# Performance work log

Hardware: AMD Instinct MI355X
Metric: run time of the kernel (lower is better)

The kernel has to match this reference:

```python
import jax, jax.numpy as jnp
import numpy as np

N, T, D, H = 256, 128, 512, 1024


def setup_inputs() -> dict:
    key = jax.random.key(0)
    k_x, k_A, k_Wx, k_Wh, k_Wa = jax.random.split(key, 5)
    x = jax.random.normal(k_x, (N, T, D), dtype=jnp.float32)
    A = jax.random.normal(k_A, (N, H, 4, 4), dtype=jnp.float32)
    Wx = jax.random.normal(k_Wx, (D, 4 * H), dtype=jnp.float32) / np.sqrt(D)
    Wh = jax.random.normal(k_Wh, (H, 4 * H), dtype=jnp.float32) / np.sqrt(H)
    Wattn = jax.random.normal(k_Wa, (H, 4 * H), dtype=jnp.float32) / np.sqrt(H)
    b = jnp.zeros((4 * H,), dtype=jnp.float32)
    return {"x": x, "A": A, "Wx": Wx, "Wh": Wh, "Wattn": Wattn, "b": b}


def _attention_lstm(x, A, Wx, Wh, Wattn, b):
    # A: (N, H, 4, 4) -> flatten spatial to (N, H, 16)
    A_flat = A.reshape(A.shape[0], A.shape[1], -1)
    h0 = A_flat.mean(axis=2)  # (N, H)
    c0 = h0
    Hdim = h0.shape[1]
    scale = 1.0 / jnp.sqrt(jnp.asarray(Hdim, dtype=x.dtype))

    def step(carry, x_t):
        prev_h, prev_c = carry
        # scaled dot-product attention over 16 spatial locations
        scores = jnp.einsum("nh,nhs->ns", prev_h, A_flat) * scale  # (N, 16)
        w = jax.nn.softmax(scores, axis=1)
        attn = jnp.einsum("nhs,ns->nh", A_flat, w)  # (N, H)
        # fused LSTM gates
        a = x_t @ Wx + prev_h @ Wh + attn @ Wattn + b  # (N, 4H)
        i = jax.nn.sigmoid(a[:, 0:Hdim])
        f = jax.nn.sigmoid(a[:, Hdim:2 * Hdim])
        o = jax.nn.sigmoid(a[:, 2 * Hdim:3 * Hdim])
        g = jnp.tanh(a[:, 3 * Hdim:4 * Hdim])
        next_c = f * prev_c + i * g
        next_h = o * jnp.tanh(next_c)
        return (next_h, next_c), next_h

    x_tnd = jnp.swapaxes(x, 0, 1)  # (T, N, D)
    _, h_tnh = jax.lax.scan(step, (h0, c0), x_tnd)
    return jnp.swapaxes(h_tnh, 0, 1)  # (N, T, H)


def reference(x, A, Wx, Wh, Wattn, b):
    return _attention_lstm(x, A, Wx, Wh, Wattn, b)
```

## Files before the change

kernel.cpp:

```cpp
#include <hip/hip_runtime.h>
#include <math.h>

#define NB 256
#define TT 128
#define DD 512
#define HH 1024
#define KHX 1536
#define KFB 2560
#define BK 128
#define NBLK7 256
#define HSLOT (NB * HH)
#define SCSLOT2 (NB * 16)

typedef _Float16 half_t;
typedef _Float16 half8 __attribute__((ext_vector_type(8)));
typedef _Float16 half4v __attribute__((ext_vector_type(4)));
typedef _Float16 half2v __attribute__((ext_vector_type(2)));
typedef float f32x4 __attribute__((ext_vector_type(4)));


__global__ __launch_bounds__(256) void k_trans(const float* __restrict__ src,
        half_t* __restrict__ dst, int kstride, int koff, int nkt) {
    __shared__ half_t tile[64][65];
    int bk = blockIdx.x % nkt;
    int bn = blockIdx.x / nkt;
    int k0 = bk * 64, n0 = bn * 64;
    #pragma unroll
    for (int i = 0; i < 16; ++i) {
        int idx = i * 256 + threadIdx.x;
        int r = idx >> 6, c = idx & 63;
        tile[c][r] = (half_t)src[(size_t)(k0 + r) * 4096 + n0 + c];
    }
    __syncthreads();
    #pragma unroll
    for (int i = 0; i < 16; ++i) {
        int idx = i * 256 + threadIdx.x;
        int r = idx >> 6, c = idx & 63;
        dst[(size_t)(n0 + r) * kstride + koff + k0 + c] = tile[r][c];
    }
}

__global__ __launch_bounds__(256) void k_convA2(const float* __restrict__ A,
        half_t* __restrict__ A16, half_t* __restrict__ AsT,
        float* __restrict__ cbuf, half_t* __restrict__ h16) {
    int n = blockIdx.x, tid = threadIdx.x;
    #pragma unroll
    for (int r = 0; r < 4; ++r) {
        int h = tid + r * 256;
        const float4* ap = (const float4*)(A + ((size_t)n * HH + h) * 16);
        float4 v0 = ap[0], v1 = ap[1], v2 = ap[2], v3 = ap[3];
        float a[16];
        a[0]=v0.x; a[1]=v0.y; a[2] =v0.z; a[3] =v0.w;
        a[4]=v1.x; a[5]=v1.y; a[6] =v1.z; a[7] =v1.w;
        a[8]=v2.x; a[9]=v2.y; a[10]=v2.z; a[11]=v2.w;
        a[12]=v3.x; a[13]=v3.y; a[14]=v3.z; a[15]=v3.w;
        float hv = 0.f;
        #pragma unroll
        for (int s = 0; s < 16; ++s) hv += a[s];
        hv *= (1.f / 16.f);
        size_t ci = (size_t)n * HH + h;
        cbuf[ci] = hv;
        h16[ci] = (half_t)hv;
        half8 q0, q1;
        #pragma unroll
        for (int s = 0; s < 8; ++s) { q0[s] = (half_t)a[s]; q1[s] = (half_t)a[s + 8]; }
        *(half8*)(A16 + ci * 16) = q0;
        *(half8*)(A16 + ci * 16 + 8) = q1;
        #pragma unroll
        for (int s = 0; s < 16; ++s)
            AsT[(size_t)n * 16 * HH + (size_t)s * HH + h] = (half_t)a[s];
    }
}

__global__ __launch_bounds__(256) void k_gemm_G(const half_t* __restrict__ AsT,
        const half_t* __restrict__ WaT, half_t* __restrict__ G16) {
    __shared__ half_t sAs[16][BK + 8];
    __shared__ half_t sB[4][16][BK + 8];
    int bid = blockIdx.x;
    int n = bid >> 6, jt = bid & 63;
    int j0 = jt * 16;
    int tid = threadIdx.x, wv = tid >> 6, lane = tid & 63;
    f32x4 acc = {};
    int srB = tid >> 2, scB = (tid & 3) * 32;
    int gB = srB >> 4, jcB = srB & 15;
    for (int it = 0; it < HH / BK; ++it) {
        int k0 = it * BK;
        if (tid < 128) {
            int r = tid >> 3, c = (tid & 7) * 16;
            const uint4* sp = (const uint4*)(AsT + (size_t)n * 16 * HH + (size_t)r * HH + k0 + c);
            uint4 u0 = sp[0], u1 = sp[1];
            *(uint4*)&sAs[r][c] = u0;
            *(uint4*)&sAs[r][c + 8] = u1;
        }
        {
            const half_t* src = WaT + ((size_t)(gB * HH + j0 + jcB)) * HH + k0 + scB;
            uint4 u0 = ((const uint4*)src)[0];
            uint4 u1 = ((const uint4*)src)[1];
            uint4 u2 = ((const uint4*)src)[2];
            uint4 u3 = ((const uint4*)src)[3];
            *((uint4*)&sB[gB][jcB][scB])      = u0;
            *((uint4*)&sB[gB][jcB][scB + 8])  = u1;
            *((uint4*)&sB[gB][jcB][scB + 16]) = u2;
            *((uint4*)&sB[gB][jcB][scB + 24]) = u3;
        }
        __syncthreads();
        int row16 = lane & 15, kg = lane >> 4;
        #pragma unroll
        for (int kc = 0; kc < BK / 32; ++kc) {
            half8 bf = *(const half8*)&sB[wv][row16][kc * 32 + kg * 8];
            half8 af = *(const half8*)&sAs[row16][kc * 32 + kg * 8];
            acc = __builtin_amdgcn_mfma_f32_16x16x32_f16(af, bf, acc, 0, 0, 0);
        }
        __syncthreads();
    }
    int col = lane & 15, rbase = (lane >> 4) * 4;
    size_t jf = (size_t)wv * HH + j0 + col;
    half4v o;
    o[0] = (half_t)acc[0]; o[1] = (half_t)acc[1];
    o[2] = (half_t)acc[2]; o[3] = (half_t)acc[3];
    *(half4v*)(G16 + ((size_t)n * 4096 + jf) * 16 + rbase) = o;
}

__global__ __launch_bounds__(256) void k_gemm_XW4(const float* __restrict__ x,
        const half_t* __restrict__ WhxT, half_t* __restrict__ XW16) {
    __shared__ half_t sA[128][72];
    __shared__ half_t sB[128][72];
    int bid = blockIdx.x;
    int bm = bid >> 5;
    int bj = bid & 31;
    int row0 = bm * 128;
    int col0 = bj * 128;
    int tid = threadIdx.x, wv = tid >> 6, lane = tid & 63;
    int la = lane & 15, kg = lane >> 4;
    int mh = wv & 1, jh = wv >> 1;
    f32x4 acc[4][4] = {};
    int rs = tid >> 1, seg = (tid & 1) * 32;
    for (int c = 0; c < 8; ++c) {
        {
            const float4* sp = (const float4*)(x + (size_t)(row0 + rs) * DD + c * 64 + seg);
            half8 p0, p1, p2, p3;
            float4 u0 = sp[0], u1 = sp[1], u2 = sp[2], u3 = sp[3];
            float4 u4 = sp[4], u5 = sp[5], u6 = sp[6], u7 = sp[7];
            p0[0]=(half_t)u0.x; p0[1]=(half_t)u0.y; p0[2]=(half_t)u0.z; p0[3]=(half_t)u0.w;
            p0[4]=(half_t)u1.x; p0[5]=(half_t)u1.y; p0[6]=(half_t)u1.z; p0[7]=(half_t)u1.w;
            p1[0]=(half_t)u2.x; p1[1]=(half_t)u2.y; p1[2]=(half_t)u2.z; p1[3]=(half_t)u2.w;
            p1[4]=(half_t)u3.x; p1[5]=(half_t)u3.y; p1[6]=(half_t)u3.z; p1[7]=(half_t)u3.w;
            p2[0]=(half_t)u4.x; p2[1]=(half_t)u4.y; p2[2]=(half_t)u4.z; p2[3]=(half_t)u4.w;
            p2[4]=(half_t)u5.x; p2[5]=(half_t)u5.y; p2[6]=(half_t)u5.z; p2[7]=(half_t)u5.w;
            p3[0]=(half_t)u6.x; p3[1]=(half_t)u6.y; p3[2]=(half_t)u6.z; p3[3]=(half_t)u6.w;
            p3[4]=(half_t)u7.x; p3[5]=(half_t)u7.y; p3[6]=(half_t)u7.z; p3[7]=(half_t)u7.w;
            *(half8*)&sA[rs][seg]      = p0;
            *(half8*)&sA[rs][seg + 8]  = p1;
            *(half8*)&sA[rs][seg + 16] = p2;
            *(half8*)&sA[rs][seg + 24] = p3;
        }
        {
            const uint4* sp = (const uint4*)(WhxT + (size_t)(col0 + rs) * KHX + c * 64 + seg);
            uint4 u0 = sp[0], u1 = sp[1];
            *(uint4*)&sB[rs][seg]     = u0;
            *(uint4*)&sB[rs][seg + 8] = u1;
        }
        __syncthreads();
        #pragma unroll
        for (int ks = 0; ks < 2; ++ks) {
            half8 bfr[4];
            #pragma unroll
            for (int jt = 0; jt < 4; ++jt)
                bfr[jt] = *(const half8*)&sB[jh * 64 + jt * 16 + la][ks * 32 + kg * 8];
            #pragma unroll
            for (int m = 0; m < 4; ++m) {
                half8 af = *(const half8*)&sA[mh * 64 + m * 16 + la][ks * 32 + kg * 8];
                #pragma unroll
                for (int jt = 0; jt < 4; ++jt)
                    acc[m][jt] = __builtin_amdgcn_mfma_f32_16x16x32_f16(af, bfr[jt], acc[m][jt], 0, 0, 0);
            }
        }
        __syncthreads();
    }
    #pragma unroll
    for (int ch = 0; ch < 2; ++ch) {
        __syncthreads();
        if (jh == ch) {
            #pragma unroll
            for (int m = 0; m < 4; ++m)
                #pragma unroll
                for (int jt = 0; jt < 4; ++jt)
                    #pragma unroll
                    for (int q = 0; q < 4; ++q)
                        sB[mh * 64 + m * 16 + kg * 4 + q][jt * 16 + la] =
                            (half_t)acc[m][jt][q];
        }
        __syncthreads();
        int cbase = col0 + ch * 64;
        int g = cbase >> 10;
        int jbb = (cbase & 1023) >> 3;
        #pragma unroll
        for (int i = 0; i < 4; ++i) {
            int idx = tid + i * 256;
            int rl = idx >> 3, grp = idx & 7;
            int R = row0 + rl;
            int t = R & 127, nn = R >> 7;
            int mh2 = nn >> 7, nl2 = nn & 127;
            size_t dst = ((((size_t)t * 128 + (jbb + grp)) * 2 + mh2) * 128 + nl2) * 32 + g * 8;
            *(half8*)(XW16 + dst) = *(const half8*)&sB[rl][grp * 8];
        }
    }
}


__global__ __launch_bounds__(512, 1) void k_steps7(
        const half_t* __restrict__ XW16, half_t* __restrict__ hh,
        const half_t* __restrict__ WhxT, const half_t* __restrict__ A16,
        const half_t* __restrict__ G16, const float* __restrict__ b,
        const float* __restrict__ cbuf, float* __restrict__ scr,
        float* __restrict__ out, int* __restrict__ bar) {
    __shared__ half_t W[32][1028];
    __shared__ float red[8][16];
    __shared__ float pe[128][33];

    int bid = blockIdx.x;
    int mhalf = bid & 1, jb = bid >> 1;
    int n0 = mhalf * 128;
    int tid = threadIdx.x;
    int wvi = tid >> 6, lane = tid & 63;
    int la = lane & 15, kg = lane >> 4;
    int* hcnt = bar + mhalf * 32;
    int* scnt = bar + 64 + mhalf * 32;

    {
        int wr = tid >> 4, seg = tid & 15;
        const half_t* wsrc = WhxT + (size_t)((wr >> 3) * HH + jb * 8 + (wr & 7)) * KHX
                           + DD + seg * 64;
        #pragma unroll
        for (int i = 0; i < 8; ++i)
            *(uint4*)&W[wr][seg * 64 + i * 8] = ((const uint4*)wsrc)[i];
    }

    int n_l = tid & 127, jg2 = tid >> 7;
    int n = n0 + n_l;
    int n_home = n0 + jb;
    int jbase = jb * 8 + jg2 * 2;
    half8 gq[4][4];
    #pragma unroll
    for (int g = 0; g < 4; ++g) {
        const half8* gsrc = (const half8*)(G16 + ((size_t)n * 4096 + g * HH + jbase) * 16);
        #pragma unroll
        for (int i = 0; i < 4; ++i) gq[g][i] = gsrc[i];
    }
    float bb[4][2];
    #pragma unroll
    for (int g = 0; g < 4; ++g) {
        bb[g][0] = b[g * HH + jbase];
        bb[g][1] = b[g * HH + jbase + 1];
    }
    float creg[2];
    creg[0] = cbuf[(size_t)n * HH + jbase];
    creg[1] = cbuf[(size_t)n * HH + jbase + 1];

    __threadfence();
    __syncthreads();

    for (int t = 0; t < TT; ++t) {
        const half_t* hcur = hh + (size_t)t * HSLOT;
        unsigned* hnext = (unsigned*)(hh + (size_t)(t + 1) * HSLOT);
        float* scw = scr + (size_t)t * SCSLOT2;

        half2v xwv[4];
        {
            const half_t* xwp = XW16 + ((((size_t)t * 128 + jb) * 2 + mhalf) * 128 + n_l) * 32;
            #pragma unroll
            for (int g = 0; g < 4; ++g) {
                unsigned u = __builtin_nontemporal_load((const unsigned*)(xwp + g * 8 + jg2 * 2));
                union { unsigned uu; half2v h2; } cv; cv.uu = u;
                xwv[g] = cv.h2;
            }
        }

        if (t > 0) {
            int tgt = 4 * t;
            int guard = 0;
            for (;;) {
                int v = (lane < 32)
                    ? __hip_atomic_load(&hcnt[lane], __ATOMIC_RELAXED, __HIP_MEMORY_SCOPE_AGENT)
                    : tgt;
                if (__all(v >= tgt)) break;
                __builtin_amdgcn_s_sleep(2);
                if (++guard > (1 << 18)) break;
            }
        }
        __builtin_amdgcn_sched_barrier(0);

        {
            half2v h2 = *(const half2v*)(hcur + (size_t)n_home * HH + 2 * tid);
            float h0 = (float)h2[0], h1 = (float)h2[1];
            const half8* ap = (const half8*)(A16 + ((size_t)n_home * HH + 2 * tid) * 16);
            half8 a0 = ap[0], a1 = ap[1], a2 = ap[2], a3 = ap[3];
            float p[16];
            #pragma unroll
            for (int s = 0; s < 8; ++s) {
                p[s]     = h0 * (float)a0[s] + h1 * (float)a2[s];
                p[s + 8] = h0 * (float)a1[s] + h1 * (float)a3[s];
            }
            #pragma unroll
            for (int off = 32; off; off >>= 1)
                #pragma unroll
                for (int s = 0; s < 16; ++s) p[s] += __shfl_xor(p[s], off, 64);
            if (lane == 0) {
                #pragma unroll
                for (int s = 0; s < 16; ++s) red[wvi][s] = p[s];
            }
        }
        __syncthreads();
        if (tid < 16) {
            float s8 = 0.f;
            #pragma unroll
            for (int w = 0; w < 8; ++w) s8 += red[w][tid];
            __hip_atomic_store(&scw[n_home * 16 + tid], s8,
                               __ATOMIC_RELAXED, __HIP_MEMORY_SCOPE_AGENT);
        }
        __syncthreads();
        if (tid == 0)
            __hip_atomic_fetch_add(&scnt[jb >> 2], 1, __ATOMIC_RELAXED,
                                   __HIP_MEMORY_SCOPE_AGENT);

        f32x4 acc0 = {}, acc1 = {};
        {
            const half_t* hrow = hcur + (size_t)(n0 + wvi * 16 + la) * HH + kg * 8;
            #pragma unroll
            for (int c = 0; c < 32; ++c) {
                half8 af = *(const half8*)(hrow + c * 32);
                half8 b0 = *(const half8*)&W[la][c * 32 + kg * 8];
                half8 b1 = *(const half8*)&W[16 + la][c * 32 + kg * 8];
                acc0 = __builtin_amdgcn_mfma_f32_16x16x32_f16(af, b0, acc0, 0, 0, 0);
                acc1 = __builtin_amdgcn_mfma_f32_16x16x32_f16(af, b1, acc1, 0, 0, 0);
            }
        }
        __syncthreads();
        #pragma unroll
        for (int q = 0; q < 4; ++q) {
            pe[wvi * 16 + kg * 4 + q][la]      = acc0[q];
            pe[wvi * 16 + kg * 4 + q][16 + la] = acc1[q];
        }
        __syncthreads();

        {
            int tgt = 4 * (t + 1);
            int guard = 0;
            for (;;) {
                int v = (lane < 32)
                    ? __hip_atomic_load(&scnt[lane], __ATOMIC_RELAXED, __HIP_MEMORY_SCOPE_AGENT)
                    : tgt;
                if (__all(v >= tgt)) break;
                __builtin_amdgcn_s_sleep(2);
                if (++guard > (1 << 18)) break;
            }
        }
        __builtin_amdgcn_sched_barrier(0);

        float w16[16];
        {
            const float4* sp = (const float4*)(scr + (size_t)t * SCSLOT2 + (size_t)n * 16);
            float4 q0 = sp[0], q1 = sp[1], q2 = sp[2], q3 = sp[3];
            float sc[16] = {q0.x, q0.y, q0.z, q0.w, q1.x, q1.y, q1.z, q1.w,
                            q2.x, q2.y, q2.z, q2.w, q3.x, q3.y, q3.z, q3.w};
            float m = -1e30f;
            #pragma unroll
            for (int s = 0; s < 16; ++s) { sc[s] *= 0.03125f; m = fmaxf(m, sc[s]); }
            float den = 0.f;
            #pragma unroll
            for (int s = 0; s < 16; ++s) { sc[s] = expf(sc[s] - m); den += sc[s]; }
            float inv = 1.f / den;
            #pragma unroll
            for (int s = 0; s < 16; ++s) w16[s] = sc[s] * inv;
        }

        float v[4][2];
        #pragma unroll
        for (int g = 0; g < 4; ++g) {
            #pragma unroll
            for (int jj = 0; jj < 2; ++jj) {
                float a0 = 0.f;
                #pragma unroll
                for (int s = 0; s < 16; ++s)
                    a0 += w16[s] * (float)gq[g][jj * 2 + (s >> 3)][s & 7];
                v[g][jj] = pe[n_l][g * 8 + jg2 * 2 + jj] + bb[g][jj]
                         + (float)xwv[g][jj] + a0;
            }
        }
        float hv[2];
        #pragma unroll
        for (int jj = 0; jj < 2; ++jj) {
            float ig = 1.f / (1.f + expf(-v[0][jj]));
            float fg = 1.f / (1.f + expf(-v[1][jj]));
            float og = 1.f / (1.f + expf(-v[2][jj]));
            float gg = tanhf(v[3][jj]);
            float cn = fg * creg[jj] + ig * gg;
            creg[jj] = cn;
            hv[jj] = og * tanhf(cn);
        }
        {
            union { float2 f2; unsigned long long u; } ov;
            ov.f2.x = hv[0]; ov.f2.y = hv[1];
            __builtin_nontemporal_store(ov.u,
                (unsigned long long*)(out + ((size_t)n * TT + t) * HH + jbase));
            union { half2v h2; unsigned u; } cv;
            cv.h2[0] = (half_t)hv[0]; cv.h2[1] = (half_t)hv[1];
            __hip_atomic_store(hnext + (((size_t)n * HH + jbase) >> 1), cv.u,
                               __ATOMIC_RELAXED, __HIP_MEMORY_SCOPE_AGENT);
        }

        __syncthreads();
        if (tid == 0)
            __hip_atomic_fetch_add(&hcnt[jb >> 2], 1, __ATOMIC_RELAXED,
                                   __HIP_MEMORY_SCOPE_AGENT);
    }
}


__global__ __launch_bounds__(256) void k_convA(const float* __restrict__ A,
        half_t* __restrict__ A16, half_t* __restrict__ AsT,
        float* __restrict__ cbuf, half_t* __restrict__ h16,
        float* __restrict__ sc0, float* __restrict__ sc1, float* __restrict__ sc2) {
    __shared__ float sred[4][16];
    int n = blockIdx.x, tid = threadIdx.x;
    float ps[16];
    #pragma unroll
    for (int s = 0; s < 16; ++s) ps[s] = 0.f;
    #pragma unroll
    for (int r = 0; r < 4; ++r) {
        int h = tid + r * 256;
        const float4* ap = (const float4*)(A + ((size_t)n * HH + h) * 16);
        float4 v0 = ap[0], v1 = ap[1], v2 = ap[2], v3 = ap[3];
        float a[16];
        a[0]=v0.x; a[1]=v0.y; a[2] =v0.z; a[3] =v0.w;
        a[4]=v1.x; a[5]=v1.y; a[6] =v1.z; a[7] =v1.w;
        a[8]=v2.x; a[9]=v2.y; a[10]=v2.z; a[11]=v2.w;
        a[12]=v3.x; a[13]=v3.y; a[14]=v3.z; a[15]=v3.w;
        float hv = 0.f;
        #pragma unroll
        for (int s = 0; s < 16; ++s) hv += a[s];
        hv *= (1.f / 16.f);
        size_t ci = (size_t)n * HH + h;
        cbuf[ci] = hv;
        h16[ci] = (half_t)hv;
        half8 q0, q1;
        #pragma unroll
        for (int s = 0; s < 8; ++s) { q0[s] = (half_t)a[s]; q1[s] = (half_t)a[s + 8]; }
        *(half8*)(A16 + ci * 16) = q0;
        *(half8*)(A16 + ci * 16 + 8) = q1;
        #pragma unroll
        for (int s = 0; s < 16; ++s)
            AsT[(size_t)n * 16 * HH + (size_t)s * HH + h] = (half_t)a[s];
        #pragma unroll
        for (int s = 0; s < 16; ++s) ps[s] += hv * a[s];
    }
    #pragma unroll
    for (int off = 32; off; off >>= 1)
        #pragma unroll
        for (int s = 0; s < 16; ++s) ps[s] += __shfl_xor(ps[s], off, 64);
    int wave = tid >> 6;
    if ((tid & 63) == 0)
        #pragma unroll
        for (int s = 0; s < 16; ++s) sred[wave][s] = ps[s];
    __syncthreads();
    if (tid < 16) {
        sc0[n * 16 + tid] = sred[0][tid] + sred[1][tid] + sred[2][tid] + sred[3][tid];
        sc1[n * 16 + tid] = 0.f;
        sc2[n * 16 + tid] = 0.f;
    }
}

union LdsS {
    struct {
        half_t sA[32][BK + 8];
        half_t sB[4][16][BK + 8];
    } s;
    float pe[4][32][16];
};

__global__ __launch_bounds__(256) void k_step(const float* __restrict__ x,
        const half_t* __restrict__ h16c, half_t* __restrict__ h16n,
        const half_t* __restrict__ WhxT, const half_t* __restrict__ A16,
        const half_t* __restrict__ G16, const float* __restrict__ b,
        float* __restrict__ cbuf, const float* __restrict__ scC,
        float* __restrict__ scN, float* __restrict__ scZ,
        float* __restrict__ out, int t) {
    __shared__ LdsS L;
    __shared__ float wlds[32][16];
    int bid = blockIdx.x;
    int xcd = bid & 7, slot = bid >> 3;
    int mtile = slot & 7, jtile = slot >> 3;
    int n0 = mtile * 32;
    int j0 = xcd * 128 + jtile * 16;
    int tid = threadIdx.x, wv = tid >> 6, lane = tid & 63;

    if (bid < 16) scZ[bid * 256 + tid] = 0.f;
    if (tid < 32) {
        int n = n0 + tid;
        const float4* sp = (const float4*)(scC + n * 16);
        float4 u0 = sp[0], u1 = sp[1], u2 = sp[2], u3 = sp[3];
        float sc[16] = {u0.x, u0.y, u0.z, u0.w, u1.x, u1.y, u1.z, u1.w,
                        u2.x, u2.y, u2.z, u2.w, u3.x, u3.y, u3.z, u3.w};
        float m = -1e30f;
        #pragma unroll
        for (int s = 0; s < 16; ++s) { sc[s] *= 0.03125f; m = fmaxf(m, sc[s]); }
        float den = 0.f;
        #pragma unroll
        for (int s = 0; s < 16; ++s) { sc[s] = expf(sc[s] - m); den += sc[s]; }
        float inv = 1.f / den;
        #pragma unroll
        for (int s = 0; s < 16; ++s) wlds[tid][s] = sc[s] * inv;
    }

    f32x4 acc[2] = {};
    int srA = tid >> 3, scA = (tid & 7) * 16;
    int srB = tid >> 2, scB = (tid & 3) * 32;
    int gB = srB >> 4, jcB = srB & 15;

    for (int it = 0; it < KHX / BK; ++it) {
        int k0 = it * BK;
        {
            int n = n0 + srA;
            if (k0 < DD) {
                const float* src = x + ((size_t)n * TT + t) * DD + k0 + scA;
                float4 v0 = ((const float4*)src)[0];
                float4 v1 = ((const float4*)src)[1];
                float4 v2 = ((const float4*)src)[2];
                float4 v3 = ((const float4*)src)[3];
                half8 p0, p1;
                p0[0] = (half_t)v0.x; p0[1] = (half_t)v0.y; p0[2] = (half_t)v0.z; p0[3] = (half_t)v0.w;
                p0[4] = (half_t)v1.x; p0[5] = (half_t)v1.y; p0[6] = (half_t)v1.z; p0[7] = (half_t)v1.w;
                p1[0] = (half_t)v2.x; p1[1] = (half_t)v2.y; p1[2] = (half_t)v2.z; p1[3] = (half_t)v2.w;
                p1[4] = (half_t)v3.x; p1[5] = (half_t)v3.y; p1[6] = (half_t)v3.z; p1[7] = (half_t)v3.w;
                *(half8*)&L.s.sA[srA][scA]     = p0;
                *(half8*)&L.s.sA[srA][scA + 8] = p1;
            } else {
                const half_t* srch = h16c + (size_t)n * HH + (k0 - DD) + scA;
                uint4 u0 = ((const uint4*)srch)[0];
                uint4 u1 = ((const uint4*)srch)[1];
                *((uint4*)&L.s.sA[srA][scA])     = u0;
                *((uint4*)&L.s.sA[srA][scA + 8]) = u1;
            }
        }
        {
            const half_t* src = WhxT + ((size_t)(gB * HH + j0 + jcB)) * KHX + k0 + scB;
            uint4 u0 = ((const uint4*)src)[0];
            uint4 u1 = ((const uint4*)src)[1];
            uint4 u2 = ((const uint4*)src)[2];
            uint4 u3 = ((const uint4*)src)[3];
            *((uint4*)&L.s.sB[gB][jcB][scB])      = u0;
            *((uint4*)&L.s.sB[gB][jcB][scB + 8])  = u1;
            *((uint4*)&L.s.sB[gB][jcB][scB + 16]) = u2;
            *((uint4*)&L.s.sB[gB][jcB][scB + 24]) = u3;
        }
        __syncthreads();
        int row16 = lane & 15, kg = lane >> 4;
        #pragma unroll
        for (int kc = 0; kc < BK / 32; ++kc) {
            half8 bf = *(const half8*)&L.s.sB[wv][row16][kc * 32 + kg * 8];
            #pragma unroll
            for (int m = 0; m < 2; ++m) {
                half8 af = *(const half8*)&L.s.sA[row16 + m * 16][kc * 32 + kg * 8];
                acc[m] = __builtin_amdgcn_mfma_f32_16x16x32_f16(af, bf, acc[m], 0, 0, 0);
            }
        }
        __syncthreads();
    }
    {
        int col = lane & 15, rbase = (lane >> 4) * 4;
        #pragma unroll
        for (int m = 0; m < 2; ++m)
            #pragma unroll
            for (int q = 0; q < 4; ++q)
                L.pe[wv][m * 16 + rbase + q][col] = acc[m][q];
    }
    __syncthreads();
    #pragma unroll
    for (int q2 = 0; q2 < 2; ++q2) {
        int idx = tid + q2 * 256;
        int r = idx >> 4, jc = idx & 15;
        int n = n0 + r, j = j0 + jc;
        float wv16[16];
        #pragma unroll
        for (int s = 0; s < 16; ++s) wv16[s] = wlds[r][s];
        float v[4];
        v[0] = L.pe[0][r][jc] + b[j];
        v[1] = L.pe[1][r][jc] + b[HH + j];
        v[2] = L.pe[2][r][jc] + b[2 * HH + j];
        v[3] = L.pe[3][r][jc] + b[3 * HH + j];
        #pragma unroll
        for (int g = 0; g < 4; ++g) {
            const half8* gq = (const half8*)(G16 + ((size_t)n * 4096 + g * HH + j) * 16);
            half8 ga = gq[0], gb2 = gq[1];
            float a0 = 0.f;
            #pragma unroll
            for (int s = 0; s < 8; ++s)
                a0 += wv16[s] * (float)ga[s] + wv16[s + 8] * (float)gb2[s];
            v[g] += a0;
        }
        float ig = 1.f / (1.f + expf(-v[0]));
        float fg = 1.f / (1.f + expf(-v[1]));
        float og = 1.f / (1.f + expf(-v[2]));
        float gg = tanhf(v[3]);
        size_t ci = (size_t)n * HH + j;
        float cp = cbuf[ci];
        float cn = fg * cp + ig * gg;
        cbuf[ci] = cn;
        float hv = og * tanhf(cn);
        out[((size_t)n * TT + t) * HH + j] = hv;
        h16n[ci] = (half_t)hv;
        const half8* ap = (const half8*)(A16 + ci * 16);
        half8 a0 = ap[0], a1 = ap[1];
        float p[16];
        #pragma unroll
        for (int s = 0; s < 8; ++s) { p[s] = hv * (float)a0[s]; p[s + 8] = hv * (float)a1[s]; }
        #pragma unroll
        for (int msk = 1; msk < 16; msk <<= 1)
            #pragma unroll
            for (int s = 0; s < 16; ++s) p[s] += __shfl_xor(p[s], msk, 64);
        float myp = 0.f;
        #pragma unroll
        for (int s = 0; s < 16; ++s) myp = (jc == s) ? p[s] : myp;
        atomicAdd(scN + n * 16 + jc, myp);
    }
}


__global__ __launch_bounds__(256) void fb_wconv(const float* __restrict__ Wx,
        const float* __restrict__ Wh, const float* __restrict__ Wa,
        half_t* __restrict__ WT) {
    __shared__ half_t tile[64][65];
    int bk = blockIdx.x % 40;
    int bn = blockIdx.x / 40;
    int k0 = bk * 64, n0 = bn * 64;
    #pragma unroll
    for (int i = 0; i < 16; ++i) {
        int idx = i * 256 + threadIdx.x;
        int r = idx >> 6, c = idx & 63;
        int k = k0 + r, n = n0 + c;
        float v;
        if (k < DD)            v = Wx[(size_t)k * 4096 + n];
        else if (k < DD + HH)  v = Wh[(size_t)(k - DD) * 4096 + n];
        else                   v = Wa[(size_t)(k - DD - HH) * 4096 + n];
        tile[c][r] = (half_t)v;
    }
    __syncthreads();
    #pragma unroll
    for (int i = 0; i < 16; ++i) {
        int idx = i * 256 + threadIdx.x;
        int r = idx >> 6, c = idx & 63;
        WT[(size_t)(n0 + r) * KFB + k0 + c] = tile[r][c];
    }
}

__global__ __launch_bounds__(256) void fb_init(const float* __restrict__ A,
        float* __restrict__ h0, float* __restrict__ c0) {
    int n = blockIdx.x;
    #pragma unroll
    for (int r = 0; r < 4; ++r) {
        int h = threadIdx.x + r * 256;
        const float4* ap = (const float4*)(A + ((size_t)n * HH + h) * 16);
        float s = 0.f;
        #pragma unroll
        for (int q = 0; q < 4; ++q) {
            float4 v = ap[q];
            s += v.x + v.y + v.z + v.w;
        }
        s *= (1.f / 16.f);
        h0[n * HH + h] = s;
        c0[n * HH + h] = s;
    }
}

__global__ __launch_bounds__(256) void fb_attn(const float* __restrict__ A,
        const float* __restrict__ hprev, long long hstride,
        half_t* __restrict__ h16, half_t* __restrict__ attn16) {
    __shared__ float sh[HH];
    __shared__ float sred[4][16];
    int n = blockIdx.x;
    const float* hp = hprev + (size_t)n * hstride;
    #pragma unroll
    for (int r = 0; r < 4; ++r) {
        int h = threadIdx.x + r * 256;
        float v = hp[h];
        sh[h] = v;
        h16[n * HH + h] = (half_t)v;
    }
    __syncthreads();
    float a[4][16];
    float ps[16];
    #pragma unroll
    for (int s = 0; s < 16; ++s) ps[s] = 0.f;
    #pragma unroll
    for (int r = 0; r < 4; ++r) {
        int h = threadIdx.x + r * 256;
        const float4* ap = (const float4*)(A + ((size_t)n * HH + h) * 16);
        float4 v0 = ap[0], v1 = ap[1], v2 = ap[2], v3 = ap[3];
        a[r][0] = v0.x;  a[r][1] = v0.y;  a[r][2]  = v0.z;  a[r][3]  = v0.w;
        a[r][4] = v1.x;  a[r][5] = v1.y;  a[r][6]  = v1.z;  a[r][7]  = v1.w;
        a[r][8] = v2.x;  a[r][9] = v2.y;  a[r][10] = v2.z;  a[r][11] = v2.w;
        a[r][12] = v3.x; a[r][13] = v3.y; a[r][14] = v3.z;  a[r][15] = v3.w;
        float hh = sh[h];
        #pragma unroll
        for (int s = 0; s < 16; ++s) ps[s] += hh * a[r][s];
    }
    #pragma unroll
    for (int off = 32; off; off >>= 1)
        #pragma unroll
        for (int s = 0; s < 16; ++s) ps[s] += __shfl_xor(ps[s], off, 64);
    int wave = threadIdx.x >> 6;
    if ((threadIdx.x & 63) == 0)
        #pragma unroll
        for (int s = 0; s < 16; ++s) sred[wave][s] = ps[s];
    __syncthreads();
    float sc[16], m = -1e30f;
    #pragma unroll
    for (int s = 0; s < 16; ++s) {
        sc[s] = (sred[0][s] + sred[1][s] + sred[2][s] + sred[3][s]) * 0.03125f;
        m = fmaxf(m, sc[s]);
    }
    float den = 0.f;
    #pragma unroll
    for (int s = 0; s < 16; ++s) { sc[s] = expf(sc[s] - m); den += sc[s]; }
    float inv = 1.f / den;
    #pragma unroll
    for (int r = 0; r < 4; ++r) {
        int h = threadIdx.x + r * 256;
        float acc = 0.f;
        #pragma unroll
        for (int s = 0; s < 16; ++s) acc += a[r][s] * sc[s];
        attn16[n * HH + h] = (half_t)(acc * inv);
    }
}

union LdsFB {
    struct {
        half_t sA[32][BK + 8];
        half_t sB[4][16][BK + 8];
    } s;
    float pe[4][32][16];
};

__global__ __launch_bounds__(256) void fb_gemm(const float* __restrict__ x,
        const half_t* __restrict__ h16, const half_t* __restrict__ attn16,
        const half_t* __restrict__ WT, const float* __restrict__ b,
        float* __restrict__ cbuf, float* __restrict__ out, int t) {
    __shared__ LdsFB L;
    int bid = blockIdx.x;
    int xcd = bid & 7;
    int slot = bid >> 3;
    int mtile = slot & 7;
    int jtile = slot >> 3;
    int m0 = mtile * 32;
    int j0 = xcd * 128 + jtile * 16;
    int tid = threadIdx.x;
    int wv = tid >> 6, lane = tid & 63;
    f32x4 acc[2] = {};
    int srA = tid >> 3, scA = (tid & 7) * 16;
    int srB = tid >> 2, scB = (tid & 3) * 32;
    int gB = srB >> 4, jcB = srB & 15;
    for (int it = 0; it < KFB / BK; ++it) {
        int k0 = it * BK;
        {
            int n = m0 + srA;
            if (k0 < DD) {
                const float* src = x + ((size_t)n * TT + t) * DD + k0 + scA;
                float4 v0 = ((const float4*)src)[0];
                float4 v1 = ((const float4*)src)[1];
                float4 v2 = ((const float4*)src)[2];
                float4 v3 = ((const float4*)src)[3];
                half8 p0, p1;
                p0[0] = (half_t)v0.x; p0[1] = (half_t)v0.y; p0[2] = (half_t)v0.z; p0[3] = (half_t)v0.w;
                p0[4] = (half_t)v1.x; p0[5] = (half_t)v1.y; p0[6] = (half_t)v1.z; p0[7] = (half_t)v1.w;
                p1[0] = (half_t)v2.x; p1[1] = (half_t)v2.y; p1[2] = (half_t)v2.z; p1[3] = (half_t)v2.w;
                p1[4] = (half_t)v3.x; p1[5] = (half_t)v3.y; p1[6] = (half_t)v3.z; p1[7] = (half_t)v3.w;
                *(half8*)&L.s.sA[srA][scA]     = p0;
                *(half8*)&L.s.sA[srA][scA + 8] = p1;
            } else {
                const half_t* srch = (k0 < DD + HH)
                    ? (h16    + (size_t)n * HH + (k0 - DD)      + scA)
                    : (attn16 + (size_t)n * HH + (k0 - DD - HH) + scA);
                uint4 u0 = ((const uint4*)srch)[0];
                uint4 u1 = ((const uint4*)srch)[1];
                *((uint4*)&L.s.sA[srA][scA])     = u0;
                *((uint4*)&L.s.sA[srA][scA + 8]) = u1;
            }
        }
        {
            const half_t* src = WT + ((size_t)(gB * HH + j0 + jcB)) * KFB + k0 + scB;
            uint4 u0 = ((const uint4*)src)[0];
            uint4 u1 = ((const uint4*)src)[1];
            uint4 u2 = ((const uint4*)src)[2];
            uint4 u3 = ((const uint4*)src)[3];
            *((uint4*)&L.s.sB[gB][jcB][scB])      = u0;
            *((uint4*)&L.s.sB[gB][jcB][scB + 8])  = u1;
            *((uint4*)&L.s.sB[gB][jcB][scB + 16]) = u2;
            *((uint4*)&L.s.sB[gB][jcB][scB + 24]) = u3;
        }
        __syncthreads();
        int row16 = lane & 15, kg = lane >> 4;
        #pragma unroll
        for (int kc = 0; kc < BK / 32; ++kc) {
            half8 bf = *(const half8*)&L.s.sB[wv][row16][kc * 32 + kg * 8];
            #pragma unroll
            for (int m = 0; m < 2; ++m) {
                half8 af = *(const half8*)&L.s.sA[row16 + m * 16][kc * 32 + kg * 8];
                acc[m] = __builtin_amdgcn_mfma_f32_16x16x32_f16(af, bf, acc[m], 0, 0, 0);
            }
        }
        __syncthreads();
    }
    {
        int col = lane & 15, rbase = (lane >> 4) * 4;
        #pragma unroll
        for (int m = 0; m < 2; ++m)
            #pragma unroll
            for (int q = 0; q < 4; ++q)
                L.pe[wv][m * 16 + rbase + q][col] = acc[m][q];
    }
    __syncthreads();
    #pragma unroll
    for (int q2 = 0; q2 < 2; ++q2) {
        int idx = tid + q2 * 256;
        int r = idx >> 4, jc = idx & 15;
        int n = m0 + r, j = j0 + jc;
        float vi = L.pe[0][r][jc] + b[j];
        float vf = L.pe[1][r][jc] + b[HH + j];
        float vo = L.pe[2][r][jc] + b[2 * HH + j];
        float vg = L.pe[3][r][jc] + b[3 * HH + j];
        float ig = 1.f / (1.f + expf(-vi));
        float fg = 1.f / (1.f + expf(-vf));
        float og = 1.f / (1.f + expf(-vo));
        float gg = tanhf(vg);
        size_t ci = (size_t)n * HH + j;
        float cp = cbuf[ci];
        float cn = fg * cp + ig * gg;
        cbuf[ci] = cn;
        out[((size_t)n * TT + t) * HH + j] = og * tanhf(cn);
    }
}


extern "C" void kernel_launch(void* const* d_in, const int* in_sizes, int n_in,
                              void* d_out, int out_size, void* d_ws, size_t ws_size,
                              hipStream_t stream) {
    const float* x  = (const float*)d_in[0];
    const float* A  = (const float*)d_in[1];
    const float* Wx = (const float*)d_in[2];
    const float* Wh = (const float*)d_in[3];
    const float* Wa = (const float*)d_in[4];
    const float* b  = (const float*)d_in[5];
    float* out = (float*)d_out;
    char* ws = (char*)d_ws;

    int maxb = 0;
    hipError_t oe = hipOccupancyMaxActiveBlocksPerMultiprocessor(&maxb, k_steps7, 512, 0);
    bool persistent_ok = (oe == hipSuccess && maxb >= 1);

    if (ws_size >= 460112128ULL && persistent_ok) {
        half_t* WhxT = (half_t*)(ws);
        half_t* WaT  = (half_t*)(ws + 12582912);
        half_t* A16  = (half_t*)(ws + 20971520);
        half_t* AsT  = (half_t*)(ws + 29360128);
        half_t* G16  = (half_t*)(ws + 37748736);
        float*  cb   = (float*) (ws + 72351744);
        int*    bar  = (int*)   (ws + 73400320);
        half_t* XW16 = (half_t*)(ws + 107004160);
        half_t* HHr  = (half_t*)(ws + 375439616);
        float*  SCr  = (float*) (ws + 443072768);

        half_t* hh0 = HHr;

        hipLaunchKernelGGL(k_trans, dim3(8 * 64),  dim3(256), 0, stream, Wx, WhxT, KHX, 0,   8);
        hipLaunchKernelGGL(k_trans, dim3(16 * 64), dim3(256), 0, stream, Wh, WhxT, KHX, 512, 16);
        hipLaunchKernelGGL(k_trans, dim3(16 * 64), dim3(256), 0, stream, Wa, WaT,  HH,  0,   16);
        hipLaunchKernelGGL(k_convA2, dim3(256), dim3(256), 0, stream, A, A16, AsT, cb, hh0);
        hipLaunchKernelGGL(k_gemm_G, dim3(NB * 64), dim3(256), 0, stream, AsT, WaT, G16);
        hipLaunchKernelGGL(k_gemm_XW4, dim3(8192), dim3(256), 0, stream, x, WhxT, XW16);
        hipMemsetAsync(bar, 0, 1024, stream);
        hipLaunchKernelGGL(k_steps7, dim3(NBLK7), dim3(512), 0, stream,
                           XW16, HHr, WhxT, A16, G16, b, cb, SCr, out, bar);
    } else if (ws_size >= 73449472ULL) {
        half_t* WhxT = (half_t*)(ws);
        half_t* WaT  = (half_t*)(ws + 12582912);
        half_t* A16  = (half_t*)(ws + 20971520);
        half_t* AsT  = (half_t*)(ws + 29360128);
        half_t* G16  = (half_t*)(ws + 37748736);
        half_t* h16a = (half_t*)(ws + 71303168);
        half_t* h16b = (half_t*)(ws + 71827456);
        float*  cb   = (float*) (ws + 72351744);
        float*  sc0  = (float*) (ws + 73400320);
        float*  sc1  = (float*) (ws + 73416704);
        float*  sc2  = (float*) (ws + 73433088);
        float* scb[3] = {sc0, sc1, sc2};

        hipLaunchKernelGGL(k_trans, dim3(8 * 64),  dim3(256), 0, stream, Wx, WhxT, KHX, 0,   8);
        hipLaunchKernelGGL(k_trans, dim3(16 * 64), dim3(256), 0, stream, Wh, WhxT, KHX, 512, 16);
        hipLaunchKernelGGL(k_trans, dim3(16 * 64), dim3(256), 0, stream, Wa, WaT,  HH,  0,   16);
        hipLaunchKernelGGL(k_convA, dim3(256), dim3(256), 0, stream,
                           A, A16, AsT, cb, h16a, sc0, sc1, sc2);
        hipLaunchKernelGGL(k_gemm_G, dim3(NB * 64), dim3(256), 0, stream, AsT, WaT, G16);
        for (int t = 0; t < TT; ++t) {
            float* scC = scb[t % 3];
            float* scN = scb[(t + 1) % 3];
            float* scZ = scb[(t + 2) % 3];
            half_t* h16c = (t & 1) ? h16b : h16a;
            half_t* h16n = (t & 1) ? h16a : h16b;
            hipLaunchKernelGGL(k_step, dim3(512), dim3(256), 0, stream,
                               x, h16c, h16n, WhxT, A16, G16, b, cb, scC, scN, scZ, out, t);
        }
    } else {
        half_t* WT  = (half_t*)ws;
        float*  h0  = (float*)(ws + 20971520);
        float*  cb  = (float*)(ws + 22020096);
        half_t* h16 = (half_t*)(ws + 23068672);
        half_t* a16 = (half_t*)(ws + 23592960);
        hipLaunchKernelGGL(fb_wconv, dim3(2560), dim3(256), 0, stream, Wx, Wh, Wa, WT);
        hipLaunchKernelGGL(fb_init, dim3(256), dim3(256), 0, stream, A, h0, cb);
        for (int t = 0; t < TT; ++t) {
            const float* hp = (t == 0) ? h0 : (out + (size_t)(t - 1) * HH);
            long long hstride = (t == 0) ? (long long)HH : (long long)TT * HH;
            hipLaunchKernelGGL(fb_attn, dim3(256), dim3(256), 0, stream, A, hp, hstride, h16, a16);
            hipLaunchKernelGGL(fb_gemm, dim3(512), dim3(256), 0, stream,
                               x, h16, a16, WT, b, cb, out, t);
        }
    }
}
```

Measured before the change: 4.627 ms.

## Repartition persistent LSTM step kernel into 8 batch groups staging h in LDS

The persistent recurrent kernel now splits the 256 blocks into 8 batch groups of 32 rows, each block covering 32 hidden columns, instead of 2 batch halves of 128 rows by 8 columns. The previous h tile is staged into shared memory once per step, and the recurrent weight slice is streamed from global memory instead of being held resident in LDS. Synchronisation is simplified to a single counter per group polled by one wave. This changes which data is reused: less h traffic per block but Wh is reread from global/L2 every step, and the single-counter atomics with 32 contenders may serialize.

```diff
diff --git a/kernel.cpp b/kernel.cpp
--- a/kernel.cpp
+++ b/kernel.cpp
@@ -8,7 +8,7 @@
 #define KHX 1536
 #define KFB 2560
 #define BK 128
-#define NBLK7 256
+#define NBLK9 256
 #define HSLOT (NB * HH)
 #define SCSLOT2 (NB * 16)
 
@@ -208,38 +208,29 @@
 }
 
 
-__global__ __launch_bounds__(512, 1) void k_steps7(
+__global__ __launch_bounds__(512, 1) void k_steps9(
         const half_t* __restrict__ XW16, half_t* __restrict__ hh,
         const half_t* __restrict__ WhxT, const half_t* __restrict__ A16,
         const half_t* __restrict__ G16, const float* __restrict__ b,
         const float* __restrict__ cbuf, float* __restrict__ scr,
         float* __restrict__ out, int* __restrict__ bar) {
-    __shared__ half_t W[32][1028];
+    __shared__ half_t sH[32][1032];
+    __shared__ float pe[32][132];
     __shared__ float red[8][16];
-    __shared__ float pe[128][33];
 
     int bid = blockIdx.x;
-    int mhalf = bid & 1, jb = bid >> 1;
-    int n0 = mhalf * 128;
+    int d = bid & 7;
+    int jb2 = bid >> 3;
+    int n0 = d * 32;
     int tid = threadIdx.x;
     int wvi = tid >> 6, lane = tid & 63;
     int la = lane & 15, kg = lane >> 4;
-    int* hcnt = bar + mhalf * 32;
-    int* scnt = bar + 64 + mhalf * 32;
-
-    {
-        int wr = tid >> 4, seg = tid & 15;
-        const half_t* wsrc = WhxT + (size_t)((wr >> 3) * HH + jb * 8 + (wr & 7)) * KHX
-                           + DD + seg * 64;
-        #pragma unroll
-        for (int i = 0; i < 8; ++i)
-            *(uint4*)&W[wr][seg * 64 + i * 8] = ((const uint4*)wsrc)[i];
-    }
-
-    int n_l = tid & 127, jg2 = tid >> 7;
+    int* hcnt = bar + d * 32;
+    int* scnt = bar + 256 + d * 32;
+
+    int n_l = tid & 31, jp = tid >> 5;
     int n = n0 + n_l;
-    int n_home = n0 + jb;
-    int jbase = jb * 8 + jg2 * 2;
+    int jbase = jb2 * 32 + jp * 2;
     half8 gq[4][4];
     #pragma unroll
     for (int g = 0; g < 4; ++g) {
@@ -256,6 +247,10 @@
     float creg[2];
     creg[0] = cbuf[(size_t)n * HH + jbase];
     creg[1] = cbuf[(size_t)n * HH + jbase + 1];
+
+    const half_t* wbase = WhxT
+        + (size_t)((wvi >> 1) * HH + jb2 * 32 + (wvi & 1) * 16 + la) * KHX
+        + DD + kg * 8;
 
     __threadfence();
     __syncthreads();
@@ -267,33 +262,41 @@
 
         half2v xwv[4];
         {
-            const half_t* xwp = XW16 + ((((size_t)t * 128 + jb) * 2 + mhalf) * 128 + n_l) * 32;
+            const half_t* xwp = XW16
+                + ((((size_t)t * 128 + (jbase >> 3)) * 2 + (n >> 7)) * 128 + (n & 127)) * 32;
             #pragma unroll
             for (int g = 0; g < 4; ++g) {
-                unsigned u = __builtin_nontemporal_load((const unsigned*)(xwp + g * 8 + jg2 * 2));
+                unsigned u = *(const unsigned*)(xwp + g * 8 + (jbase & 7));
                 union { unsigned uu; half2v h2; } cv; cv.uu = u;
                 xwv[g] = cv.h2;
             }
         }
 
         if (t > 0) {
-            int tgt = 4 * t;
-            int guard = 0;
-            for (;;) {
-                int v = (lane < 32)
-                    ? __hip_atomic_load(&hcnt[lane], __ATOMIC_RELAXED, __HIP_MEMORY_SCOPE_AGENT)
-                    : tgt;
-                if (__all(v >= tgt)) break;
-                __builtin_amdgcn_s_sleep(2);
-                if (++guard > (1 << 18)) break;
-            }
-        }
-        __builtin_amdgcn_sched_barrier(0);
-
-        {
-            half2v h2 = *(const half2v*)(hcur + (size_t)n_home * HH + 2 * tid);
-            float h0 = (float)h2[0], h1 = (float)h2[1];
-            const half8* ap = (const half8*)(A16 + ((size_t)n_home * HH + 2 * tid) * 16);
+            if (wvi == 0) {
+                int tgt = 32 * t, guard = 0;
+                while (__hip_atomic_load(hcnt, __ATOMIC_RELAXED,
+                                         __HIP_MEMORY_SCOPE_AGENT) < tgt) {
+                    __builtin_amdgcn_s_sleep(2);
+                    if (++guard > (1 << 20)) break;
+                }
+            }
+            __syncthreads();
+        }
+
+        {
+            int r = tid >> 4, cseg = (tid & 15) * 64;
+            const uint4* sp = (const uint4*)(hcur + (size_t)(n0 + r) * HH + cseg);
+            #pragma unroll
+            for (int i = 0; i < 8; ++i)
+                *(uint4*)&sH[r][cseg + i * 8] = sp[i];
+        }
+        __syncthreads();
+
+        {
+            float h0 = (float)sH[jb2][2 * tid];
+            float h1 = (float)sH[jb2][2 * tid + 1];
+            const half8* ap = (const half8*)(A16 + ((size_t)(n0 + jb2) * HH + 2 * tid) * 16);
             half8 a0 = ap[0], a1 = ap[1], a2 = ap[2], a3 = ap[3];
             float p[16];
             #pragma unroll
@@ -315,51 +318,44 @@
             float s8 = 0.f;
             #pragma unroll
             for (int w = 0; w < 8; ++w) s8 += red[w][tid];
-            __hip_atomic_store(&scw[n_home * 16 + tid], s8,
+            __hip_atomic_store(&scw[(size_t)(n0 + jb2) * 16 + tid], s8,
                                __ATOMIC_RELAXED, __HIP_MEMORY_SCOPE_AGENT);
         }
         __syncthreads();
         if (tid == 0)
-            __hip_atomic_fetch_add(&scnt[jb >> 2], 1, __ATOMIC_RELAXED,
+            __hip_atomic_fetch_add(scnt, 1, __ATOMIC_RELAXED,
                                    __HIP_MEMORY_SCOPE_AGENT);
 
         f32x4 acc0 = {}, acc1 = {};
-        {
-            const half_t* hrow = hcur + (size_t)(n0 + wvi * 16 + la) * HH + kg * 8;
-            #pragma unroll
-            for (int c = 0; c < 32; ++c) {
-                half8 af = *(const half8*)(hrow + c * 32);
-                half8 b0 = *(const half8*)&W[la][c * 32 + kg * 8];
-                half8 b1 = *(const half8*)&W[16 + la][c * 32 + kg * 8];
-                acc0 = __builtin_amdgcn_mfma_f32_16x16x32_f16(af, b0, acc0, 0, 0, 0);
-                acc1 = __builtin_amdgcn_mfma_f32_16x16x32_f16(af, b1, acc1, 0, 0, 0);
-            }
+        #pragma unroll 4
+        for (int c = 0; c < 32; ++c) {
+            half8 bf = *(const half8*)(wbase + c * 32);
+            half8 a0 = *(const half8*)&sH[la][c * 32 + kg * 8];
+            half8 a1 = *(const half8*)&sH[16 + la][c * 32 + kg * 8];
+            acc0 = __builtin_amdgcn_mfma_f32_16x16x32_f16(a0, bf, acc0, 0, 0, 0);
+            acc1 = __builtin_amdgcn_mfma_f32_16x16x32_f16(a1, bf, acc1, 0, 0, 0);
         }
         __syncthreads();
         #pragma unroll
         for (int q = 0; q < 4; ++q) {
-            pe[wvi * 16 + kg * 4 + q][la]      = acc0[q];
-            pe[wvi * 16 + kg * 4 + q][16 + la] = acc1[q];
-        }
-        __syncthreads();
-
-        {
-            int tgt = 4 * (t + 1);
-            int guard = 0;
-            for (;;) {
-                int v = (lane < 32)
-                    ? __hip_atomic_load(&scnt[lane], __ATOMIC_RELAXED, __HIP_MEMORY_SCOPE_AGENT)
-                    : tgt;
-                if (__all(v >= tgt)) break;
+            pe[kg * 4 + q][wvi * 16 + la]      = acc0[q];
+            pe[16 + kg * 4 + q][wvi * 16 + la] = acc1[q];
+        }
+        __syncthreads();
+
+        if (wvi == 0) {
+            int tgt = 32 * (t + 1), guard = 0;
+            while (__hip_atomic_load(scnt, __ATOMIC_RELAXED,
+                                     __HIP_MEMORY_SCOPE_AGENT) < tgt) {
                 __builtin_amdgcn_s_sleep(2);
-                if (++guard > (1 << 18)) break;
-            }
-        }
-        __builtin_amdgcn_sched_barrier(0);
+                if (++guard > (1 << 20)) break;
+            }
+        }
+        __syncthreads();
 
         float w16[16];
         {
-            const float4* sp = (const float4*)(scr + (size_t)t * SCSLOT2 + (size_t)n * 16);
+            const float4* sp = (const float4*)(scw + (size_t)n * 16);
             float4 q0 = sp[0], q1 = sp[1], q2 = sp[2], q3 = sp[3];
             float sc[16] = {q0.x, q0.y, q0.z, q0.w, q1.x, q1.y, q1.z, q1.w,
                             q2.x, q2.y, q2.z, q2.w, q3.x, q3.y, q3.z, q3.w};
@@ -383,7 +379,7 @@
                 #pragma unroll
                 for (int s = 0; s < 16; ++s)
                     a0 += w16[s] * (float)gq[g][jj * 2 + (s >> 3)][s & 7];
-                v[g][jj] = pe[n_l][g * 8 + jg2 * 2 + jj] + bb[g][jj]
+                v[g][jj] = pe[n_l][g * 32 + jp * 2 + jj] + bb[g][jj]
                          + (float)xwv[g][jj] + a0;
             }
         }
@@ -399,10 +395,8 @@
             hv[jj] = og * tanhf(cn);
         }
         {
-            union { float2 f2; unsigned long long u; } ov;
-            ov.f2.x = hv[0]; ov.f2.y = hv[1];
-            __builtin_nontemporal_store(ov.u,
-                (unsigned long long*)(out + ((size_t)n * TT + t) * HH + jbase));
+            float2 o2; o2.x = hv[0]; o2.y = hv[1];
+            *(float2*)(out + ((size_t)n * TT + t) * HH + jbase) = o2;
             union { half2v h2; unsigned u; } cv;
             cv.h2[0] = (half_t)hv[0]; cv.h2[1] = (half_t)hv[1];
             __hip_atomic_store(hnext + (((size_t)n * HH + jbase) >> 1), cv.u,
@@ -411,7 +405,7 @@
 
         __syncthreads();
         if (tid == 0)
-            __hip_atomic_fetch_add(&hcnt[jb >> 2], 1, __ATOMIC_RELAXED,
+            __hip_atomic_fetch_add(hcnt, 1, __ATOMIC_RELAXED,
                                    __HIP_MEMORY_SCOPE_AGENT);
     }
 }
@@ -854,7 +848,7 @@
     char* ws = (char*)d_ws;
 
     int maxb = 0;
-    hipError_t oe = hipOccupancyMaxActiveBlocksPerMultiprocessor(&maxb, k_steps7, 512, 0);
+    hipError_t oe = hipOccupancyMaxActiveBlocksPerMultiprocessor(&maxb, k_steps9, 512, 0);
     bool persistent_ok = (oe == hipSuccess && maxb >= 1);
 
     if (ws_size >= 460112128ULL && persistent_ok) {
@@ -877,8 +871,8 @@
         hipLaunchKernelGGL(k_convA2, dim3(256), dim3(256), 0, stream, A, A16, AsT, cb, hh0);
         hipLaunchKernelGGL(k_gemm_G, dim3(NB * 64), dim3(256), 0, stream, AsT, WaT, G16);
         hipLaunchKernelGGL(k_gemm_XW4, dim3(8192), dim3(256), 0, stream, x, WhxT, XW16);
-        hipMemsetAsync(bar, 0, 1024, stream);
-        hipLaunchKernelGGL(k_steps7, dim3(NBLK7), dim3(512), 0, stream,
+        hipMemsetAsync(bar, 0, 2048, stream);
+        hipLaunchKernelGGL(k_steps9, dim3(NBLK9), dim3(512), 0, stream,
                            XW16, HHr, WhxT, A16, G16, b, cb, SCr, out, bar);
     } else if (ws_size >= 73449472ULL) {
         half_t* WhxT = (half_t*)(ws);
```

Result: no change. 4.644 ms (+0.4%).
